# Kernel optimization log

Measured on AMD Instinct MI355X. Metric: run time of the kernel, lower is better.

## Reference

```python
import jax, jax.numpy as jnp
import numpy as np
from jax import lax

T, B, IN, H = 500, 32, 512, 1024


def hard_sigmoid(x):
    # torch version reduces to clip(0.2*x + 0.5, 0, 1)
    return jnp.clip(0.2 * x + 0.5, 0.0, 1.0)


def hard_tanh(x):
    return jnp.clip(x, -1.0, 1.0)


def setup_inputs() -> dict:
    key = jax.random.key(0)
    ks = jax.random.split(key, 9)
    stdv = 1.0 / np.sqrt(H)
    u = lambda k, shp: jax.random.uniform(k, shp, jnp.float32, -stdv, stdv)
    return {
        "x": jax.random.normal(ks[0], (T, B, IN), jnp.float32),
        "w_ih_f": u(ks[1], (4 * H, IN)),
        "w_hh_f": u(ks[2], (4 * H, H)),
        "b_ih_f": u(ks[3], (4 * H,)),
        "b_hh_f": u(ks[4], (4 * H,)),
        "w_ih_r": u(ks[5], (4 * H, IN)),
        "w_hh_r": u(ks[6], (4 * H, H)),
        "b_ih_r": u(ks[7], (4 * H,)),
        "b_hh_r": u(ks[8], (4 * H,)),
    }


def _run_direction(x, w_ih, w_hh, b_ih, b_hh, reverse):
    # Precompute input projection for all timesteps in one big GEMM: [T,B,4H]
    gx = jnp.einsum('tbi,gi->tbg', x, w_ih) + b_ih + b_hh
    if reverse:
        gx = gx[::-1]
    h0 = jnp.zeros((x.shape[1], w_hh.shape[1]), x.dtype)
    c0 = jnp.zeros_like(h0)

    def step(carry, g):
        h, c = carry
        gates = g + h @ w_hh.T  # [B,4H]
        i, f, cg, o = jnp.split(gates, 4, axis=-1)
        i = hard_sigmoid(i)
        f = hard_sigmoid(f)
        cg = hard_tanh(cg)
        o = hard_sigmoid(o)
        c = f * c + i * cg
        h = o * hard_tanh(c)
        return (h, c), h

    (h, c), ys = lax.scan(step, (h0, c0), gx)
    if reverse:
        ys = ys[::-1]
    return ys, h, c


def reference(x, w_ih_f, w_hh_f, b_ih_f, b_hh_f, w_ih_r, w_hh_r, b_ih_r, b_hh_r):
    out_f, h_f, c_f = _run_direction(x, w_ih_f, w_hh_f, b_ih_f, b_hh_f, False)
    out_r, h_r, c_r = _run_direction(x, w_ih_r, w_hh_r, b_ih_r, b_hh_r, True)
    output = jnp.concatenate([out_f, out_r], axis=-1)  # [T,B,2H]
    hy = jnp.stack([h_f, h_r], axis=0)  # [2,B,H]
    cy = jnp.stack([c_f, c_r], axis=0)
    return output, (hy, cy)
```

## Files before the change

kernel.cpp:

```cpp
#include <hip/hip_runtime.h>

#define T_   500
#define B_   32
#define IN_  512
#define H_   1024
#define NWG  128
#define NPD  64
#define THR  512

typedef _Float16 f16x8 __attribute__((ext_vector_type(8)));
typedef float    f32x4 __attribute__((ext_vector_type(4)));

#define MFMA __builtin_amdgcn_mfma_f32_16x16x32_f16

#define WAITV(N) do { asm volatile("s_waitcnt vmcnt(" #N ")" ::: "memory"); \
                      __builtin_amdgcn_sched_barrier(0); } while (0)

#define HLOAD(r, ks) \
  asm volatile("global_load_dwordx4 %0, %1, off offset:%2 sc0 sc1" \
               : "=v"(hf##r) : "v"(aH), "i"(64 * (ks)) : "memory")

#define HSTEP(r, ks) do { \
  const int t_ = (kq512 + (ks) * 64 + fkb16) ^ sw; \
  acc0 = MFMA(hf##r, *(const f16x8*)(WhB0 + t_), acc0, 0, 0, 0); \
  acc1 = MFMA(hf##r, *(const f16x8*)(WhB1 + t_), acc1, 0, 0, 0); \
  acc2 = MFMA(hf##r, *(const f16x8*)(WhB2 + t_), acc2, 0, 0, 0); \
  acc3 = MFMA(hf##r, *(const f16x8*)(WhB3 + t_), acc3, 0, 0, 0); } while (0)

__device__ __forceinline__ f16x8 cvt8(float4 lo, float4 hi) {
  return (f16x8){ (_Float16)lo.x, (_Float16)lo.y, (_Float16)lo.z, (_Float16)lo.w,
                  (_Float16)hi.x, (_Float16)hi.y, (_Float16)hi.z, (_Float16)hi.w };
}

__global__ void cvt_x_kernel(const float* __restrict__ x, _Float16* __restrict__ xb, int n8) {
  int i = blockIdx.x * blockDim.x + threadIdx.x;
  if (i >= n8) return;
  const float4* p = (const float4*)x + (size_t)i * 2;
  *((f16x8*)xb + i) = cvt8(p[0], p[1]);
}

__global__ __launch_bounds__(THR, 1) void lstm_kernel(
    const float* __restrict__ w_ih_f, const float* __restrict__ w_hh_f,
    const float* __restrict__ b_ih_f, const float* __restrict__ b_hh_f,
    const float* __restrict__ w_ih_r, const float* __restrict__ w_hh_r,
    const float* __restrict__ b_ih_r, const float* __restrict__ b_hh_r,
    const _Float16* __restrict__ xb, _Float16* __restrict__ hb,
    unsigned* __restrict__ flags, float* __restrict__ out)
{
  __shared__ _Float16 Wh[64 * 1024];
  __shared__ float    pg[4][32][64];

  const int wg   = blockIdx.x;
  const int dir  = wg >> 6;
  const int slot = wg & 63;
  const int col0 = slot * 16;
  const int tid  = threadIdx.x;

  const float* w_ih = dir ? w_ih_r : w_ih_f;
  const float* w_hh = dir ? w_hh_r : w_hh_f;
  const float* b_ih = dir ? b_ih_r : b_ih_f;
  const float* b_hh = dir ? b_hh_r : b_hh_f;

  unsigned* fl = flags + dir * NPD;

  for (int i = tid; i < 64 * 128; i += THR) {
    const int r  = i >> 7;
    const int k  = (i & 127) * 8;
    const int gr = (r >> 4) * H_ + col0 + (r & 15);
    const float4* p = (const float4*)(w_hh + (size_t)gr * H_ + k);
    const int byte = r * 2048 + ((k * 2) ^ ((r & 7) << 4));
    *(f16x8*)((char*)Wh + byte) = cvt8(p[0], p[1]);
  }

  const int lane = tid & 63, wv = tid >> 6;
  const int mh = wv & 1, kq = wv >> 1;
  const int frow = lane & 15, fkb = lane >> 4;
  const int mrow = mh * 16 + frow;
  const int sw    = (frow & 7) << 4;
  const int kq512 = kq * 512;
  const int fkb16 = fkb * 16;
  const char* WhB0 = (const char*)Wh + (size_t)( 0 + frow) * 2048;
  const char* WhB1 = (const char*)Wh + (size_t)(16 + frow) * 2048;
  const char* WhB2 = (const char*)Wh + (size_t)(32 + frow) * 2048;
  const char* WhB3 = (const char*)Wh + (size_t)(48 + frow) * 2048;

  f16x8 xw0[4], xw1[4], xw2[4], xw3[4];
#pragma unroll
  for (int ks = 0; ks < 4; ++ks) {
    const int k = kq * 128 + ks * 32 + fkb * 8;
    { const float4* p = (const float4*)(w_ih + (size_t)(0 * H_ + col0 + frow) * IN_ + k);
      xw0[ks] = cvt8(p[0], p[1]); }
    { const float4* p = (const float4*)(w_ih + (size_t)(1 * H_ + col0 + frow) * IN_ + k);
      xw1[ks] = cvt8(p[0], p[1]); }
    { const float4* p = (const float4*)(w_ih + (size_t)(2 * H_ + col0 + frow) * IN_ + k);
      xw2[ks] = cvt8(p[0], p[1]); }
    { const float4* p = (const float4*)(w_ih + (size_t)(3 * H_ + col0 + frow) * IN_ + k);
      xw3[ks] = cvt8(p[0], p[1]); }
  }

  const int tb = tid >> 4, thc = tid & 15, tcol = col0 + thc;
  const float b0 = b_ih[0 * H_ + tcol] + b_hh[0 * H_ + tcol];
  const float b1 = b_ih[1 * H_ + tcol] + b_hh[1 * H_ + tcol];
  const float b2 = b_ih[2 * H_ + tcol] + b_hh[2 * H_ + tcol];
  const float b3 = b_ih[3 * H_ + tcol] + b_hh[3 * H_ + tcol];
  float c = 0.f;

  const size_t hbase = (size_t)(dir * 2) * B_ * H_;

  __syncthreads();

  for (int s = 0; s < T_; ++s) {
    const int tx = dir ? (T_ - 1 - s) : s;

    const _Float16* aX = xb + ((size_t)tx * B_ + mrow) * IN_ + kq * 128 + fkb * 8;
    f32x4 acc0 = {0,0,0,0}, acc1 = {0,0,0,0}, acc2 = {0,0,0,0}, acc3 = {0,0,0,0};
#pragma unroll
    for (int ks = 0; ks < 4; ++ks) {
      f16x8 xa = *(const f16x8*)(aX + ks * 32);
      acc0 = MFMA(xa, xw0[ks], acc0, 0, 0, 0);
      acc1 = MFMA(xa, xw1[ks], acc1, 0, 0, 0);
      acc2 = MFMA(xa, xw2[ks], acc2, 0, 0, 0);
      acc3 = MFMA(xa, xw3[ks], acc3, 0, 0, 0);
    }
    __builtin_amdgcn_sched_barrier(0);

    if (s > 0) {
      if (wv == 0) {
        const unsigned tgt = (unsigned)s;
        int guard = 0;
        for (;;) {
          unsigned f = __hip_atomic_load(fl + lane, __ATOMIC_RELAXED, __HIP_MEMORY_SCOPE_AGENT);
          if (__all(f >= tgt)) break;
          __builtin_amdgcn_s_sleep(1);
          if (++guard > (1 << 22)) break;
        }
      }
      __syncthreads();
      asm volatile("" ::: "memory");

      const _Float16* aH = hb + hbase + (size_t)((s & 1) * B_ + mrow) * H_ + kq * 256 + fkb * 8;
      f16x8 hf0, hf1, hf2, hf3, hf4, hf5, hf6, hf7;
      HLOAD(0, 0); HLOAD(1, 1); HLOAD(2, 2); HLOAD(3, 3);
      HLOAD(4, 4); HLOAD(5, 5); HLOAD(6, 6); HLOAD(7, 7);
      WAITV(4);
      HSTEP(0, 0); HSTEP(1, 1); HSTEP(2, 2); HSTEP(3, 3);
      WAITV(0);
      HSTEP(4, 4); HSTEP(5, 5); HSTEP(6, 6); HSTEP(7, 7);
    }

#pragma unroll
    for (int i = 0; i < 4; ++i) {
      const int m = mh * 16 + fkb * 4 + i;
      pg[kq][m][ 0 + frow] = acc0[i];
      pg[kq][m][16 + frow] = acc1[i];
      pg[kq][m][32 + frow] = acc2[i];
      pg[kq][m][48 + frow] = acc3[i];
    }
    __syncthreads();

    float xi = pg[0][tb][ 0 + thc] + pg[1][tb][ 0 + thc] + pg[2][tb][ 0 + thc] + pg[3][tb][ 0 + thc] + b0;
    float xf = pg[0][tb][16 + thc] + pg[1][tb][16 + thc] + pg[2][tb][16 + thc] + pg[3][tb][16 + thc] + b1;
    float xg = pg[0][tb][32 + thc] + pg[1][tb][32 + thc] + pg[2][tb][32 + thc] + pg[3][tb][32 + thc] + b2;
    float xo = pg[0][tb][48 + thc] + pg[1][tb][48 + thc] + pg[2][tb][48 + thc] + pg[3][tb][48 + thc] + b3;
    float ig = fminf(fmaxf(0.2f * xi + 0.5f, 0.f), 1.f);
    float fg = fminf(fmaxf(0.2f * xf + 0.5f, 0.f), 1.f);
    float cg = fminf(fmaxf(xg, -1.f), 1.f);
    float og = fminf(fmaxf(0.2f * xo + 0.5f, 0.f), 1.f);
    c = fg * c + ig * cg;
    float hv = og * fminf(fmaxf(c, -1.f), 1.f);

    out[((size_t)tx * B_ + tb) * (2 * H_) + dir * H_ + tcol] = hv;
    {
      const _Float16* hp = hb + hbase + (size_t)(((s + 1) & 1) * B_ + tb) * H_ + tcol;
      unsigned hbits = (unsigned)__builtin_bit_cast(unsigned short, (_Float16)hv);
      asm volatile("global_store_short %0, %1, off sc0 sc1" :: "v"(hp), "v"(hbits) : "memory");
    }
    if (s == T_ - 1) {
      const size_t HY = (size_t)T_ * B_ * 2 * H_;
      out[HY + ((size_t)dir * B_ + tb) * H_ + tcol] = hv;
      out[HY + (size_t)2 * B_ * H_ + ((size_t)dir * B_ + tb) * H_ + tcol] = c;
    }

    asm volatile("s_waitcnt vmcnt(0)" ::: "memory");
    __syncthreads();
    if (tid == 0)
      __hip_atomic_store(fl + slot, (unsigned)(s + 1), __ATOMIC_RELAXED, __HIP_MEMORY_SCOPE_AGENT);
  }
}

extern "C" void kernel_launch(void* const* d_in, const int* in_sizes, int n_in,
                              void* d_out, int out_size, void* d_ws, size_t ws_size,
                              hipStream_t stream) {
  const float* x      = (const float*)d_in[0];
  const float* w_ih_f = (const float*)d_in[1];
  const float* w_hh_f = (const float*)d_in[2];
  const float* b_ih_f = (const float*)d_in[3];
  const float* b_hh_f = (const float*)d_in[4];
  const float* w_ih_r = (const float*)d_in[5];
  const float* w_hh_r = (const float*)d_in[6];
  const float* b_ih_r = (const float*)d_in[7];
  const float* b_hh_r = (const float*)d_in[8];
  float* out = (float*)d_out;

  char* ws = (char*)d_ws;
  _Float16* xb    = (_Float16*)ws;
  _Float16* hb    = (_Float16*)(ws + 16384000);
  unsigned* flags = (unsigned*)(ws + 16384000 + 262144);

  hipMemsetAsync(flags, 0, 1024, stream);
  cvt_x_kernel<<<4000, 256, 0, stream>>>(x, xb, 1024000);
  lstm_kernel<<<NWG, THR, 0, stream>>>(w_ih_f, w_hh_f, b_ih_f, b_hh_f,
                                       w_ih_r, w_hh_r, b_ih_r, b_hh_r,
                                       xb, hb, flags, out);
}
```

Measured before the change: 2.314 ms.

## Replace per-step flag barrier with step-tagged hidden-state words polled directly

```diff
diff --git a/kernel.cpp b/kernel.cpp
--- a/kernel.cpp
+++ b/kernel.cpp
@@ -16,16 +16,26 @@
 #define WAITV(N) do { asm volatile("s_waitcnt vmcnt(" #N ")" ::: "memory"); \
                       __builtin_amdgcn_sched_barrier(0); } while (0)
 
-#define HLOAD(r, ks) \
-  asm volatile("global_load_dwordx4 %0, %1, off offset:%2 sc0 sc1" \
-               : "=v"(hf##r) : "v"(aH), "i"(64 * (ks)) : "memory")
-
-#define HSTEP(r, ks) do { \
+#define PISS(r, off) do { if (!(done & (1u << (r)))) \
+  asm volatile("global_load_dwordx4 %0, %1, off offset:" #off " sc0 sc1" \
+               : "=v"(q##r) : "v"(aH) : "memory"); } while (0)
+
+#define PCHK(r) do { if (!(done & (1u << (r)))) { \
+  unsigned bad_ = ((q##r.x ^ tagw) | (q##r.y ^ tagw) | (q##r.z ^ tagw) | (q##r.w ^ tagw)) \
+                  & 0xFFFF0000u; \
+  if (bad_ == 0u) done |= (1u << (r)); } } while (0)
+
+#define HPACK(dst, qa, qb) do { \
+  uint4 t_ = { (qa.x & 0xFFFFu) | (qa.y << 16), (qa.z & 0xFFFFu) | (qa.w << 16), \
+               (qb.x & 0xFFFFu) | (qb.y << 16), (qb.z & 0xFFFFu) | (qb.w << 16) }; \
+  dst = __builtin_bit_cast(f16x8, t_); } while (0)
+
+#define HSTEP(hf, ks) do { \
   const int t_ = (kq512 + (ks) * 64 + fkb16) ^ sw; \
-  acc0 = MFMA(hf##r, *(const f16x8*)(WhB0 + t_), acc0, 0, 0, 0); \
-  acc1 = MFMA(hf##r, *(const f16x8*)(WhB1 + t_), acc1, 0, 0, 0); \
-  acc2 = MFMA(hf##r, *(const f16x8*)(WhB2 + t_), acc2, 0, 0, 0); \
-  acc3 = MFMA(hf##r, *(const f16x8*)(WhB3 + t_), acc3, 0, 0, 0); } while (0)
+  acc0 = MFMA(hf, *(const f16x8*)(WhB0 + t_), acc0, 0, 0, 0); \
+  acc1 = MFMA(hf, *(const f16x8*)(WhB1 + t_), acc1, 0, 0, 0); \
+  acc2 = MFMA(hf, *(const f16x8*)(WhB2 + t_), acc2, 0, 0, 0); \
+  acc3 = MFMA(hf, *(const f16x8*)(WhB3 + t_), acc3, 0, 0, 0); } while (0)
 
 __device__ __forceinline__ f16x8 cvt8(float4 lo, float4 hi) {
   return (f16x8){ (_Float16)lo.x, (_Float16)lo.y, (_Float16)lo.z, (_Float16)lo.w,
@@ -44,8 +54,8 @@
     const float* __restrict__ b_ih_f, const float* __restrict__ b_hh_f,
     const float* __restrict__ w_ih_r, const float* __restrict__ w_hh_r,
     const float* __restrict__ b_ih_r, const float* __restrict__ b_hh_r,
-    const _Float16* __restrict__ xb, _Float16* __restrict__ hb,
-    unsigned* __restrict__ flags, float* __restrict__ out)
+    const _Float16* __restrict__ xb, unsigned* __restrict__ hbw,
+    float* __restrict__ out)
 {
   __shared__ _Float16 Wh[64 * 1024];
   __shared__ float    pg[4][32][64];
@@ -60,8 +70,6 @@
   const float* w_hh = dir ? w_hh_r : w_hh_f;
   const float* b_ih = dir ? b_ih_r : b_ih_f;
   const float* b_hh = dir ? b_hh_r : b_hh_f;
-
-  unsigned* fl = flags + dir * NPD;
 
   for (int i = tid; i < 64 * 128; i += THR) {
     const int r  = i >> 7;
@@ -105,8 +113,6 @@
   const float b3 = b_ih[3 * H_ + tcol] + b_hh[3 * H_ + tcol];
   float c = 0.f;
 
-  const size_t hbase = (size_t)(dir * 2) * B_ * H_;
-
   __syncthreads();
 
   for (int s = 0; s < T_; ++s) {
@@ -122,30 +128,37 @@
       acc2 = MFMA(xa, xw2[ks], acc2, 0, 0, 0);
       acc3 = MFMA(xa, xw3[ks], acc3, 0, 0, 0);
     }
-    __builtin_amdgcn_sched_barrier(0);
 
     if (s > 0) {
-      if (wv == 0) {
-        const unsigned tgt = (unsigned)s;
-        int guard = 0;
-        for (;;) {
-          unsigned f = __hip_atomic_load(fl + lane, __ATOMIC_RELAXED, __HIP_MEMORY_SCOPE_AGENT);
-          if (__all(f >= tgt)) break;
-          __builtin_amdgcn_s_sleep(1);
-          if (++guard > (1 << 22)) break;
-        }
+      const unsigned* aH = hbw + ((size_t)(dir * 2 + (s & 1)) * B_ + mrow) * H_
+                               + kq * 256 + fkb * 8;
+      const unsigned tagw = (unsigned)s << 16;
+      uint4 q0, q1, q2, q3, q4, q5, q6, q7, q8, q9, q10, q11, q12, q13, q14, q15;
+      unsigned done = 0;
+      int guard = 0;
+      for (;;) {
+        PISS( 0,   0); PISS( 1,  16); PISS( 2, 128); PISS( 3, 144);
+        PISS( 4, 256); PISS( 5, 272); PISS( 6, 384); PISS( 7, 400);
+        PISS( 8, 512); PISS( 9, 528); PISS(10, 640); PISS(11, 656);
+        PISS(12, 768); PISS(13, 784); PISS(14, 896); PISS(15, 912);
+        WAITV(0);
+        PCHK( 0); PCHK( 1); PCHK( 2); PCHK( 3);
+        PCHK( 4); PCHK( 5); PCHK( 6); PCHK( 7);
+        PCHK( 8); PCHK( 9); PCHK(10); PCHK(11);
+        PCHK(12); PCHK(13); PCHK(14); PCHK(15);
+        if (__all(done == 0xFFFFu)) break;
+        if (++guard > (1 << 16)) break;
       }
-      __syncthreads();
-      asm volatile("" ::: "memory");
-
-      const _Float16* aH = hb + hbase + (size_t)((s & 1) * B_ + mrow) * H_ + kq * 256 + fkb * 8;
-      f16x8 hf0, hf1, hf2, hf3, hf4, hf5, hf6, hf7;
-      HLOAD(0, 0); HLOAD(1, 1); HLOAD(2, 2); HLOAD(3, 3);
-      HLOAD(4, 4); HLOAD(5, 5); HLOAD(6, 6); HLOAD(7, 7);
-      WAITV(4);
-      HSTEP(0, 0); HSTEP(1, 1); HSTEP(2, 2); HSTEP(3, 3);
-      WAITV(0);
-      HSTEP(4, 4); HSTEP(5, 5); HSTEP(6, 6); HSTEP(7, 7);
+
+      f16x8 hf;
+      HPACK(hf, q0,  q1 ); HSTEP(hf, 0);
+      HPACK(hf, q2,  q3 ); HSTEP(hf, 1);
+      HPACK(hf, q4,  q5 ); HSTEP(hf, 2);
+      HPACK(hf, q6,  q7 ); HSTEP(hf, 3);
+      HPACK(hf, q8,  q9 ); HSTEP(hf, 4);
+      HPACK(hf, q10, q11); HSTEP(hf, 5);
+      HPACK(hf, q12, q13); HSTEP(hf, 6);
+      HPACK(hf, q14, q15); HSTEP(hf, 7);
     }
 
 #pragma unroll
@@ -170,10 +183,12 @@
     float hv = og * fminf(fmaxf(c, -1.f), 1.f);
 
     out[((size_t)tx * B_ + tb) * (2 * H_) + dir * H_ + tcol] = hv;
+
     {
-      const _Float16* hp = hb + hbase + (size_t)(((s + 1) & 1) * B_ + tb) * H_ + tcol;
-      unsigned hbits = (unsigned)__builtin_bit_cast(unsigned short, (_Float16)hv);
-      asm volatile("global_store_short %0, %1, off sc0 sc1" :: "v"(hp), "v"(hbits) : "memory");
+      unsigned hword = (unsigned)__builtin_bit_cast(unsigned short, (_Float16)hv)
+                     | ((unsigned)(s + 1) << 16);
+      unsigned* hp = hbw + ((size_t)(dir * 2 + ((s + 1) & 1)) * B_ + tb) * H_ + tcol;
+      asm volatile("global_store_dword %0, %1, off sc0 sc1" :: "v"(hp), "v"(hword) : "memory");
     }
     if (s == T_ - 1) {
       const size_t HY = (size_t)T_ * B_ * 2 * H_;
@@ -181,10 +196,7 @@
       out[HY + (size_t)2 * B_ * H_ + ((size_t)dir * B_ + tb) * H_ + tcol] = c;
     }
 
-    asm volatile("s_waitcnt vmcnt(0)" ::: "memory");
     __syncthreads();
-    if (tid == 0)
-      __hip_atomic_store(fl + slot, (unsigned)(s + 1), __ATOMIC_RELAXED, __HIP_MEMORY_SCOPE_AGENT);
   }
 }
 
@@ -203,13 +215,12 @@
   float* out = (float*)d_out;
 
   char* ws = (char*)d_ws;
-  _Float16* xb    = (_Float16*)ws;
-  _Float16* hb    = (_Float16*)(ws + 16384000);
-  unsigned* flags = (unsigned*)(ws + 16384000 + 262144);
-
-  hipMemsetAsync(flags, 0, 1024, stream);
+  _Float16* xb  = (_Float16*)ws;
+  unsigned* hbw = (unsigned*)(ws + 16384000);
+
+  hipMemsetAsync(hbw, 0, 524288, stream);
   cvt_x_kernel<<<4000, 256, 0, stream>>>(x, xb, 1024000);
   lstm_kernel<<<NWG, THR, 0, stream>>>(w_ih_f, w_hh_f, b_ih_f, b_hh_f,
                                        w_ih_r, w_hh_r, b_ih_r, b_hh_r,
-                                       xb, hb, flags, out);
-}
+                                       xb, hbw, out);
+}
```

After: 3.209 ms. 38.7% more time.

## Prefetch x tile before the flag wait and defer flag publish to the next step

Applied to the files above, without the earlier changes.

```diff
diff --git a/kernel.cpp b/kernel.cpp
--- a/kernel.cpp
+++ b/kernel.cpp
@@ -16,9 +16,17 @@
 #define WAITV(N) do { asm volatile("s_waitcnt vmcnt(" #N ")" ::: "memory"); \
                       __builtin_amdgcn_sched_barrier(0); } while (0)
 
-#define HLOAD(r, ks) \
-  asm volatile("global_load_dwordx4 %0, %1, off offset:%2 sc0 sc1" \
-               : "=v"(hf##r) : "v"(aH), "i"(64 * (ks)) : "memory")
+#define XLOAD(r, ks) asm volatile("global_load_dwordx4 %0, %1, off offset:%2" \
+  : "=v"(xa##r) : "v"(aX), "i"(64*(ks)) : "memory")
+
+#define HLOAD(r, ks) asm volatile("global_load_dwordx4 %0, %1, off offset:%2 sc0 sc1" \
+  : "=v"(hf##r) : "v"(aH), "i"(64*(ks)) : "memory")
+
+#define XSTEP(r, ks) do { \
+  acc0 = MFMA(xa##r, xw0[ks], acc0, 0, 0, 0); \
+  acc1 = MFMA(xa##r, xw1[ks], acc1, 0, 0, 0); \
+  acc2 = MFMA(xa##r, xw2[ks], acc2, 0, 0, 0); \
+  acc3 = MFMA(xa##r, xw3[ks], acc3, 0, 0, 0); } while (0)
 
 #define HSTEP(r, ks) do { \
   const int t_ = (kq512 + (ks) * 64 + fkb16) ^ sw; \
@@ -113,18 +121,16 @@
     const int tx = dir ? (T_ - 1 - s) : s;
 
     const _Float16* aX = xb + ((size_t)tx * B_ + mrow) * IN_ + kq * 128 + fkb * 8;
-    f32x4 acc0 = {0,0,0,0}, acc1 = {0,0,0,0}, acc2 = {0,0,0,0}, acc3 = {0,0,0,0};
-#pragma unroll
-    for (int ks = 0; ks < 4; ++ks) {
-      f16x8 xa = *(const f16x8*)(aX + ks * 32);
-      acc0 = MFMA(xa, xw0[ks], acc0, 0, 0, 0);
-      acc1 = MFMA(xa, xw1[ks], acc1, 0, 0, 0);
-      acc2 = MFMA(xa, xw2[ks], acc2, 0, 0, 0);
-      acc3 = MFMA(xa, xw3[ks], acc3, 0, 0, 0);
-    }
-    __builtin_amdgcn_sched_barrier(0);
-
+    f16x8 xa0, xa1, xa2, xa3;
+    XLOAD(0, 0); XLOAD(1, 1); XLOAD(2, 2); XLOAD(3, 3);
+
+    f16x8 hf0, hf1, hf2, hf3, hf4, hf5, hf6, hf7;
     if (s > 0) {
+      WAITV(4);
+      __builtin_amdgcn_s_barrier();
+      if (tid == 0)
+        __hip_atomic_store(fl + slot, (unsigned)s, __ATOMIC_RELAXED, __HIP_MEMORY_SCOPE_AGENT);
+
       if (wv == 0) {
         const unsigned tgt = (unsigned)s;
         int guard = 0;
@@ -135,13 +141,21 @@
           if (++guard > (1 << 22)) break;
         }
       }
-      __syncthreads();
+      __builtin_amdgcn_s_barrier();
       asm volatile("" ::: "memory");
 
       const _Float16* aH = hb + hbase + (size_t)((s & 1) * B_ + mrow) * H_ + kq * 256 + fkb * 8;
-      f16x8 hf0, hf1, hf2, hf3, hf4, hf5, hf6, hf7;
       HLOAD(0, 0); HLOAD(1, 1); HLOAD(2, 2); HLOAD(3, 3);
       HLOAD(4, 4); HLOAD(5, 5); HLOAD(6, 6); HLOAD(7, 7);
+      WAITV(8);
+    } else {
+      WAITV(0);
+    }
+
+    f32x4 acc0 = {0,0,0,0}, acc1 = {0,0,0,0}, acc2 = {0,0,0,0}, acc3 = {0,0,0,0};
+    XSTEP(0, 0); XSTEP(1, 1); XSTEP(2, 2); XSTEP(3, 3);
+
+    if (s > 0) {
       WAITV(4);
       HSTEP(0, 0); HSTEP(1, 1); HSTEP(2, 2); HSTEP(3, 3);
       WAITV(0);
@@ -156,7 +170,9 @@
       pg[kq][m][32 + frow] = acc2[i];
       pg[kq][m][48 + frow] = acc3[i];
     }
-    __syncthreads();
+    asm volatile("s_waitcnt lgkmcnt(0)" ::: "memory");
+    __builtin_amdgcn_s_barrier();
+    __builtin_amdgcn_sched_barrier(0);
 
     float xi = pg[0][tb][ 0 + thc] + pg[1][tb][ 0 + thc] + pg[2][tb][ 0 + thc] + pg[3][tb][ 0 + thc] + b0;
     float xf = pg[0][tb][16 + thc] + pg[1][tb][16 + thc] + pg[2][tb][16 + thc] + pg[3][tb][16 + thc] + b1;
@@ -169,7 +185,10 @@
     c = fg * c + ig * cg;
     float hv = og * fminf(fmaxf(c, -1.f), 1.f);
 
-    out[((size_t)tx * B_ + tb) * (2 * H_) + dir * H_ + tcol] = hv;
+    {
+      float* op = out + ((size_t)tx * B_ + tb) * (2 * H_) + dir * H_ + tcol;
+      asm volatile("global_store_dword %0, %1, off" :: "v"(op), "v"(hv) : "memory");
+    }
     {
       const _Float16* hp = hb + hbase + (size_t)(((s + 1) & 1) * B_ + tb) * H_ + tcol;
       unsigned hbits = (unsigned)__builtin_bit_cast(unsigned short, (_Float16)hv);
@@ -180,11 +199,6 @@
       out[HY + ((size_t)dir * B_ + tb) * H_ + tcol] = hv;
       out[HY + (size_t)2 * B_ * H_ + ((size_t)dir * B_ + tb) * H_ + tcol] = c;
     }
-
-    asm volatile("s_waitcnt vmcnt(0)" ::: "memory");
-    __syncthreads();
-    if (tid == 0)
-      __hip_atomic_store(fl + slot, (unsigned)(s + 1), __ATOMIC_RELAXED, __HIP_MEMORY_SCOPE_AGENT);
   }
 }
 
```

Result: slower. 3.223 ms (+39.3%).
